# Kernel tuning notes

Measured on AMD Instinct MI355X. Metric: run time of the kernel, lower is better.

The kernel has to match this reference:

```python
import jax, jax.numpy as jnp
import numpy as np

UNITS = 50
FEAT = 128
OUT = 74


def _glorot(key, shape):
    fan_in, fan_out = shape[0], shape[1]
    lim = (6.0 / (fan_in + fan_out)) ** 0.5
    return jax.random.uniform(key, shape, jnp.float32, -lim, lim)


def setup_inputs() -> dict:
    key = jax.random.key(0)
    ks = jax.random.split(key, 8)
    x = jax.random.normal(ks[0], (1024, 256, FEAT), jnp.float32)
    # forward-direction LSTM params (keras gate order: i, f, c, o)
    W_f = _glorot(ks[1], (FEAT, 4 * UNITS))
    U_f = _glorot(ks[2], (UNITS, 4 * UNITS))
    b_f = jnp.zeros((4 * UNITS,), jnp.float32).at[UNITS:2 * UNITS].set(1.0)  # unit forget bias
    # backward-direction LSTM params
    W_b = _glorot(ks[3], (FEAT, 4 * UNITS))
    U_b = _glorot(ks[4], (UNITS, 4 * UNITS))
    b_b = jnp.zeros((4 * UNITS,), jnp.float32).at[UNITS:2 * UNITS].set(1.0)
    # dense softmax head: [2*UNITS, OUT]
    W_d = _glorot(ks[5], (2 * UNITS, OUT))
    b_d = jnp.zeros((OUT,), jnp.float32)
    return {"x": x, "W_f": W_f, "U_f": U_f, "b_f": b_f,
            "W_b": W_b, "U_b": U_b, "b_b": b_b, "W_d": W_d, "b_d": b_d}


def _lstm_last(x, W, U, b):
    # x: [B, T, F]; relu cell activation, sigmoid recurrent activation (keras defaults except activation)
    B = x.shape[0]
    h0 = jnp.zeros((B, UNITS), x.dtype)
    c0 = jnp.zeros((B, UNITS), x.dtype)
    # precompute input projections for all timesteps: [T, B, 4U]
    zx = jnp.einsum('btf,fg->tbg', x, W) + b

    def step(carry, zx_t):
        h, c = carry
        z = zx_t + h @ U
        i, f, g, o = jnp.split(z, 4, axis=-1)
        i = jax.nn.sigmoid(i)
        f = jax.nn.sigmoid(f)
        g = jax.nn.relu(g)
        o = jax.nn.sigmoid(o)
        c = f * c + i * g
        h = o * jax.nn.relu(c)
        return (h, c), None

    (h, c), _ = jax.lax.scan(step, (h0, c0), zx)
    return h  # last hidden state, [B, UNITS]


def reference(x, W_f, U_f, b_f, W_b, U_b, b_b, W_d, b_d):
    h_fwd = _lstm_last(x, W_f, U_f, b_f)
    h_bwd = _lstm_last(x[:, ::-1, :], W_b, U_b, b_b)
    h = jnp.concatenate([h_fwd, h_bwd], axis=-1)  # [B, 100]
    logits = h @ W_d + b_d
    return jax.nn.softmax(logits, axis=-1)  # [B, 74]
```

## Files before the change

### kernel.cpp

```cpp
#include <hip/hip_runtime.h>
#include <hip/hip_bf16.h>
#include <math.h>

#define T_SEQ 256
#define FEAT  128
#define UNITS 50
#define NG    200
#define OUTD  74
#define BATCH 1024
#define NPAD  224
#define WPLANE (NPAD * FEAT)

typedef __attribute__((ext_vector_type(8)))  short bf16x8;
typedef __attribute__((ext_vector_type(16))) float f32x16;

__device__ __forceinline__ unsigned short f2bf(float f) {
    unsigned u = __float_as_uint(f);
    return (unsigned short)((u + 0x7fffu + ((u >> 16) & 1u)) >> 16);
}
__device__ __forceinline__ float bf2f(unsigned short h) {
    return __uint_as_float(((unsigned)h) << 16);
}
__device__ __forceinline__ float sigf(float x) {
    return __builtin_amdgcn_rcpf(1.f + __expf(-x));
}

__global__ __launch_bounds__(256) void prep_w(
    const float* __restrict__ Wf, const float* __restrict__ Wb,
    unsigned short* __restrict__ Wt)
{
    const int idx = blockIdx.x * 256 + threadIdx.x;
    const int dir = blockIdx.y;
    const int col = idx >> 7, k = idx & 127;
    const float* W = dir ? Wb : Wf;
    const float v = (col < NG) ? W[k * NG + col] : 0.f;
    const unsigned short hi = f2bf(v);
    const unsigned short lo = f2bf(v - bf2f(hi));
    Wt[(size_t)(dir * 2 + 0) * WPLANE + idx] = hi;
    Wt[(size_t)(dir * 2 + 1) * WPLANE + idx] = lo;
}

__global__ __launch_bounds__(256) void prep_x(
    const float* __restrict__ x,
    unsigned short* __restrict__ xh, unsigned short* __restrict__ xl,
    int Tc, int lTc, int t0, int n4)
{
    const int stride = gridDim.x * blockDim.x;
    for (int e4 = blockIdx.x * blockDim.x + threadIdx.x; e4 < n4; e4 += stride) {
        const int row = e4 >> 5, k4 = e4 & 31;
        const int b = row >> lTc, ti = row & (Tc - 1);
        const float4 v = *(const float4*)(x + (((size_t)(b * T_SEQ + t0 + ti)) << 7) + (k4 << 2));
        ushort4 hi, lo;
        hi.x = f2bf(v.x); lo.x = f2bf(v.x - bf2f(hi.x));
        hi.y = f2bf(v.y); lo.y = f2bf(v.y - bf2f(hi.y));
        hi.z = f2bf(v.z); lo.z = f2bf(v.z - bf2f(hi.z));
        hi.w = f2bf(v.w); lo.w = f2bf(v.w - bf2f(hi.w));
        *(ushort4*)(xh + ((size_t)e4 << 2)) = hi;
        *(ushort4*)(xl + ((size_t)e4 << 2)) = lo;
    }
}

__global__ __launch_bounds__(448, 2) void proj_mfma(
    const unsigned short* __restrict__ xfh, const unsigned short* __restrict__ xfl,
    const unsigned short* __restrict__ xbh, const unsigned short* __restrict__ xbl,
    const unsigned short* __restrict__ Wt,
    float* __restrict__ zf, float* __restrict__ zb,
    int mpb, int nMT)
{
    const int dir = blockIdx.y;
    const unsigned short* __restrict__ Ah_p = dir ? xbh : xfh;
    const unsigned short* __restrict__ Al_p = dir ? xbl : xfl;
    float* __restrict__ z = dir ? zb : zf;
    const unsigned short* __restrict__ Wth = Wt + (size_t)(dir * 2) * WPLANE;
    const unsigned short* __restrict__ Wtl = Wth + WPLANE;

    const int l    = threadIdx.x & 63;
    const int wv   = threadIdx.x >> 6;
    const int ln   = l & 31;
    const int half = l >> 5;
    const int col  = wv * 32 + ln;

    bf16x8 Bh[8], Bl[8];
#pragma unroll
    for (int ks = 0; ks < 8; ++ks) {
        const size_t wo = (size_t)col * 128 + ks * 16 + half * 8;
        Bh[ks] = *(const bf16x8*)(Wth + wo);
        Bl[ks] = *(const bf16x8*)(Wtl + wo);
    }
    const bool colOK = (col < NG);

    int mt = blockIdx.x * mpb;
    bf16x8 Ah[8], Al[8], Ah2[8], Al2[8];
    {
        const size_t ab = ((size_t)(mt * 32 + ln)) << 7;
#pragma unroll
        for (int ks = 0; ks < 8; ++ks) {
            Ah[ks] = *(const bf16x8*)(Ah_p + ab + ks * 16 + half * 8);
            Al[ks] = *(const bf16x8*)(Al_p + ab + ks * 16 + half * 8);
        }
    }

    for (int i = 0; i < mpb; ++i) {
        const int mtn = (i + 1 < mpb) ? (mt + 1) : mt;
        const size_t an = ((size_t)(mtn * 32 + ln)) << 7;
#pragma unroll
        for (int ks = 0; ks < 8; ++ks) {
            Ah2[ks] = *(const bf16x8*)(Ah_p + an + ks * 16 + half * 8);
            Al2[ks] = *(const bf16x8*)(Al_p + an + ks * 16 + half * 8);
        }

        f32x16 acc = {};
#pragma unroll
        for (int ks = 0; ks < 8; ++ks) {
            acc = __builtin_amdgcn_mfma_f32_32x32x16_bf16(Ah[ks], Bh[ks], acc, 0, 0, 0);
            acc = __builtin_amdgcn_mfma_f32_32x32x16_bf16(Ah[ks], Bl[ks], acc, 0, 0, 0);
            acc = __builtin_amdgcn_mfma_f32_32x32x16_bf16(Al[ks], Bh[ks], acc, 0, 0, 0);
        }

        if (colOK) {
            float* zp = z + (size_t)(mt * 32 + half * 4) * NG + col;
#pragma unroll
            for (int r = 0; r < 16; ++r) {
                const int row = (r & 3) + ((r >> 2) << 3);
                zp[(size_t)row * NG] = acc[r];
            }
        }
#pragma unroll
        for (int ks = 0; ks < 8; ++ks) { Ah[ks] = Ah2[ks]; Al[ks] = Al2[ks]; }
        ++mt;
    }
}

__global__ __launch_bounds__(256, 4) void rec3(
    const float* __restrict__ zf, const float* __restrict__ zb,
    const float* __restrict__ Uf, const float* __restrict__ Ub,
    const float* __restrict__ bf_, const float* __restrict__ bb_,
    float* __restrict__ hF, float* __restrict__ cF,
    float* __restrict__ hB, float* __restrict__ cB,
    int Tc, int first)
{
    const int j = threadIdx.x;
    const int b = blockIdx.x, dir = blockIdx.y;
    const float* __restrict__ z    = dir ? zb : zf;
    const float* __restrict__ U    = dir ? Ub : Uf;
    const float* __restrict__ bias = dir ? bb_ : bf_;
    float* __restrict__ hS = dir ? hB : hF;
    float* __restrict__ cS = dir ? cB : cF;
    const bool act = (j < NG);
    const bool isg = (j >= 100) && (j < 150);

    float Ur[50];
#pragma unroll
    for (int k = 0; k < 50; ++k) Ur[k] = act ? U[k * NG + j] : 0.f;
    const float bj = act ? bias[j] : 0.f;

    __shared__ __align__(16) float hsh[52];
    __shared__ float gsh[NG];

    float c = 0.f;
    if (j < 50) {
        c      = first ? 0.f : cS[b * 50 + j];
        hsh[j] = first ? 0.f : hS[b * 50 + j];
    }
    if (j >= 50 && j < 52) hsh[j] = 0.f;
    __syncthreads();

    const int stp = dir ? -1 : 1;
    int ti = dir ? (Tc - 1) : 0;
    const float* __restrict__ zr = z + (size_t)b * Tc * NG;

    float zc = act ? zr[(size_t)ti * NG + j] : 0.f;

    for (int tt = 0; tt < Tc; ++tt) {
        const int tin = ti + stp;
        float zn = 0.f;
        if (tt + 1 < Tc && act) zn = zr[(size_t)tin * NG + j];

        float a = zc + bj;
#pragma unroll
        for (int k4 = 0; k4 < 12; ++k4) {
            const float4 h4 = *(const float4*)(hsh + (k4 << 2));
            a = fmaf(h4.x, Ur[k4 * 4 + 0], a);
            a = fmaf(h4.y, Ur[k4 * 4 + 1], a);
            a = fmaf(h4.z, Ur[k4 * 4 + 2], a);
            a = fmaf(h4.w, Ur[k4 * 4 + 3], a);
        }
        {
            const float2 h2 = *(const float2*)(hsh + 48);
            a = fmaf(h2.x, Ur[48], a);
            a = fmaf(h2.y, Ur[49], a);
        }

        const float s = sigf(a);
        const float r = fmaxf(a, 0.f);
        if (act) gsh[j] = isg ? r : s;
        __syncthreads();

        if (j < 50) {
            const float gi = gsh[j];
            const float gf = gsh[50 + j];
            const float gg = gsh[100 + j];
            const float go = gsh[150 + j];
            c = fmaf(gf, c, gi * gg);
            hsh[j] = go * fmaxf(c, 0.f);
        }
        __syncthreads();

        zc = zn;
        ti = tin;
    }

    if (j < 50) {
        hS[b * 50 + j] = hsh[j];
        cS[b * 50 + j] = c;
    }
}

__global__ __launch_bounds__(128) void head_kernel(
    const float* __restrict__ hF, const float* __restrict__ hB,
    const float* __restrict__ Wd, const float* __restrict__ bd,
    float* __restrict__ out)
{
    const int b   = blockIdx.x;
    const int tid = threadIdx.x;
    __shared__ float hsh[100];
    __shared__ float red[128];

    if (tid < 50) {
        hsh[tid]      = hF[b * 50 + tid];
        hsh[50 + tid] = hB[b * 50 + tid];
    }
    __syncthreads();

    float logit = -INFINITY;
    if (tid < OUTD) {
        float acc = bd[tid];
#pragma unroll 4
        for (int k = 0; k < 100; ++k) acc = fmaf(hsh[k], Wd[k * OUTD + tid], acc);
        logit = acc;
    }
    red[tid] = logit;
    __syncthreads();
    for (int s = 64; s > 0; s >>= 1) {
        if (tid < s) red[tid] = fmaxf(red[tid], red[tid + s]);
        __syncthreads();
    }
    const float m = red[0];
    __syncthreads();
    const float e = (tid < OUTD) ? expf(logit - m) : 0.f;
    red[tid] = e;
    __syncthreads();
    for (int s = 64; s > 0; s >>= 1) {
        if (tid < s) red[tid] += red[tid + s];
        __syncthreads();
    }
    if (tid < OUTD) out[b * OUTD + tid] = e / red[0];
}

extern "C" void kernel_launch(void* const* d_in, const int* in_sizes, int n_in,
                              void* d_out, int out_size, void* d_ws, size_t ws_size,
                              hipStream_t stream)
{
    const float* x  = (const float*)d_in[0];
    const float* Wf = (const float*)d_in[1];
    const float* Uf = (const float*)d_in[2];
    const float* bf = (const float*)d_in[3];
    const float* Wb = (const float*)d_in[4];
    const float* Ub = (const float*)d_in[5];
    const float* bb = (const float*)d_in[6];
    const float* Wd = (const float*)d_in[7];
    const float* bd = (const float*)d_in[8];
    float* out = (float*)d_out;

    auto aln = [](size_t v) { return (v + 255) & ~(size_t)255; };

    int Tc = T_SEQ;
    bool shx = true;
    for (;;) {
        shx = (Tc == T_SEQ);
        const size_t zsz = aln((size_t)BATCH * Tc * NG * 4);
        const size_t xsz = aln((size_t)BATCH * Tc * FEAT * 2);
        const size_t need = 2 * zsz + (shx ? 2 : 4) * xsz
                          + aln(4 * WPLANE * 2) + aln(4ull * BATCH * UNITS * 4);
        if (need <= ws_size || Tc == 8) break;
        Tc >>= 1;
    }
    const int lTc = __builtin_ctz((unsigned)Tc);
    const size_t zsz = aln((size_t)BATCH * Tc * NG * 4);
    const size_t xsz = aln((size_t)BATCH * Tc * FEAT * 2);

    char* p = (char*)d_ws;
    float* zf = (float*)p; p += zsz;
    float* zb = (float*)p; p += zsz;
    unsigned short* xfh = (unsigned short*)p; p += xsz;
    unsigned short* xfl = (unsigned short*)p; p += xsz;
    unsigned short* xbh = xfh;
    unsigned short* xbl = xfl;
    if (!shx) {
        xbh = (unsigned short*)p; p += xsz;
        xbl = (unsigned short*)p; p += xsz;
    }
    unsigned short* Wt = (unsigned short*)p; p += aln(4 * WPLANE * 2);
    float* st = (float*)p;
    float* hF = st;
    float* cF = st + BATCH * UNITS;
    float* hB = st + 2 * BATCH * UNITS;
    float* cB = st + 3 * BATCH * UNITS;

    prep_w<<<dim3(WPLANE / 256, 2), 256, 0, stream>>>(Wf, Wb, Wt);

    const int n4  = BATCH * Tc * 32;
    const int nMT = BATCH * Tc / 32;
    const int NBLK = (nMT < 512) ? nMT : 512;
    const int mpb = nMT / NBLK;
    const int nc  = T_SEQ / Tc;

    for (int c = 0; c < nc; ++c) {
        const int t0f = c * Tc;
        const int t0b = T_SEQ - (c + 1) * Tc;
        prep_x<<<2048, 256, 0, stream>>>(x, xfh, xfl, Tc, lTc, t0f, n4);
        if (!shx)
            prep_x<<<2048, 256, 0, stream>>>(x, xbh, xbl, Tc, lTc, t0b, n4);
        proj_mfma<<<dim3(NBLK, 2), 448, 0, stream>>>(
            xfh, xfl, xbh, xbl, Wt, zf, zb, mpb, nMT);
        rec3<<<dim3(BATCH, 2), 256, 0, stream>>>(
            zf, zb, Uf, Ub, bf, bb, hF, cF, hB, cB, Tc, c == 0);
    }
    head_kernel<<<BATCH, 128, 0, stream>>>(hF, hB, Wd, bd, out);
}
```

Baseline: 944.3 us.

## Batch recurrent LSTM step over 32 sequences using split-bf16 MFMA

The recurrent kernel is replaced: each block now handles 32 batch rows per direction instead of one. The h·U product runs on 32x32x16 bf16 MFMAs, using a hi/lo split with three products per k-slice to stay close to fp32 accuracy. U is pre-split into bf16 planes by a new prep kernel, and h is kept in LDS as bf16 hi/lo pairs. This removes per-sequence scalar FMA loops and amortises U loads, but the grid shrinks to 64 blocks, which leaves most CUs idle during the latency-bound time loop.

```diff
diff --git a/kernel.cpp b/kernel.cpp
--- a/kernel.cpp
+++ b/kernel.cpp
@@ -10,6 +10,11 @@
 #define BATCH 1024
 #define NPAD  224
 #define WPLANE (NPAD * FEAT)
+#define G32   32
+#define KP    64
+#define HL    68
+#define GSW   224
+#define UPLANE (NPAD * KP)
 
 typedef __attribute__((ext_vector_type(8)))  short bf16x8;
 typedef __attribute__((ext_vector_type(16))) float f32x16;
@@ -38,6 +43,21 @@
     const unsigned short lo = f2bf(v - bf2f(hi));
     Wt[(size_t)(dir * 2 + 0) * WPLANE + idx] = hi;
     Wt[(size_t)(dir * 2 + 1) * WPLANE + idx] = lo;
+}
+
+__global__ __launch_bounds__(256) void prep_u(
+    const float* __restrict__ Uf, const float* __restrict__ Ub,
+    unsigned short* __restrict__ Ut)
+{
+    const int idx = blockIdx.x * 256 + threadIdx.x;
+    const int dir = blockIdx.y;
+    const int col = idx >> 6, k = idx & 63;
+    const float* U = dir ? Ub : Uf;
+    const float v = (col < NG && k < UNITS) ? U[k * NG + col] : 0.f;
+    const unsigned short hi = f2bf(v);
+    const unsigned short lo = f2bf(v - bf2f(hi));
+    Ut[(size_t)(dir * 2 + 0) * UPLANE + idx] = hi;
+    Ut[(size_t)(dir * 2 + 1) * UPLANE + idx] = lo;
 }
 
 __global__ __launch_bounds__(256) void prep_x(
@@ -131,88 +151,156 @@
     }
 }
 
-__global__ __launch_bounds__(256, 4) void rec3(
+__global__ __launch_bounds__(512, 1) void rec4(
     const float* __restrict__ zf, const float* __restrict__ zb,
-    const float* __restrict__ Uf, const float* __restrict__ Ub,
+    const unsigned short* __restrict__ Ut,
     const float* __restrict__ bf_, const float* __restrict__ bb_,
     float* __restrict__ hF, float* __restrict__ cF,
     float* __restrict__ hB, float* __restrict__ cB,
     int Tc, int first)
 {
-    const int j = threadIdx.x;
-    const int b = blockIdx.x, dir = blockIdx.y;
+    const int tid = threadIdx.x;
+    const int dir = blockIdx.y;
+    const int b0  = blockIdx.x * G32;
     const float* __restrict__ z    = dir ? zb : zf;
-    const float* __restrict__ U    = dir ? Ub : Uf;
     const float* __restrict__ bias = dir ? bb_ : bf_;
+    const unsigned short* __restrict__ Uth = Ut + (size_t)(dir * 2) * UPLANE;
+    const unsigned short* __restrict__ Utl = Uth + UPLANE;
     float* __restrict__ hS = dir ? hB : hF;
     float* __restrict__ cS = dir ? cB : cF;
-    const bool act = (j < NG);
-    const bool isg = (j >= 100) && (j < 150);
-
-    float Ur[50];
-#pragma unroll
-    for (int k = 0; k < 50; ++k) Ur[k] = act ? U[k * NG + j] : 0.f;
-    const float bj = act ? bias[j] : 0.f;
-
-    __shared__ __align__(16) float hsh[52];
-    __shared__ float gsh[NG];
-
-    float c = 0.f;
-    if (j < 50) {
-        c      = first ? 0.f : cS[b * 50 + j];
-        hsh[j] = first ? 0.f : hS[b * 50 + j];
-    }
-    if (j >= 50 && j < 52) hsh[j] = 0.f;
-    __syncthreads();
-
+
+    __shared__ unsigned short h_hi[G32][HL];
+    __shared__ unsigned short h_lo[G32][HL];
+    __shared__ float gsh[G32][GSW];
+
+    const int l    = tid & 63;
+    const int wv   = tid >> 6;
+    const int ln   = l & 31;
+    const int half = l >> 5;
+    const int col  = wv * 32 + ln;
+    const bool mf  = (wv < 7);
+    const bool cOK = mf && (col < NG);
+    const bool isg = (col >= 100) && (col < 150);
+    const float bcol = cOK ? bias[col] : 0.f;
+
+    bf16x8 Bh0 = {}, Bh1 = {}, Bh2 = {}, Bh3 = {};
+    bf16x8 Bl0 = {}, Bl1 = {}, Bl2 = {}, Bl3 = {};
+    if (mf) {
+        const size_t ob = (size_t)col * KP + half * 8;
+        Bh0 = *(const bf16x8*)(Uth + ob);      Bl0 = *(const bf16x8*)(Utl + ob);
+        Bh1 = *(const bf16x8*)(Uth + ob + 16); Bl1 = *(const bf16x8*)(Utl + ob + 16);
+        Bh2 = *(const bf16x8*)(Uth + ob + 32); Bl2 = *(const bf16x8*)(Utl + ob + 32);
+        Bh3 = *(const bf16x8*)(Uth + ob + 48); Bl3 = *(const bf16x8*)(Utl + ob + 48);
+    }
+
+    for (int idx = tid; idx < G32 * HL; idx += 512) {
+        ((unsigned short*)h_hi)[idx] = 0;
+        ((unsigned short*)h_lo)[idx] = 0;
+    }
+    __syncthreads();
+    float creg[4] = {0.f, 0.f, 0.f, 0.f};
+#pragma unroll
+    for (int i = 0; i < 4; ++i) {
+        const int m = tid + i * 512;
+        if (m < G32 * UNITS && !first) {
+            const int r = m / UNITS, u = m % UNITS;
+            creg[i] = cS[(b0 + r) * UNITS + u];
+            const float hv = hS[(b0 + r) * UNITS + u];
+            const unsigned short hi = f2bf(hv);
+            h_hi[r][u] = hi;
+            h_lo[r][u] = f2bf(hv - bf2f(hi));
+        }
+    }
+    __syncthreads();
+
+    unsigned zrb[16];
+    if (cOK) {
+#pragma unroll
+        for (int i = 0; i < 16; ++i) {
+            const int row = (i & 3) + ((i >> 2) << 3) + half * 4;
+            zrb[i] = (unsigned)(((b0 + row) * Tc) * NG + col);
+        }
+    }
     const int stp = dir ? -1 : 1;
-    int ti = dir ? (Tc - 1) : 0;
-    const float* __restrict__ zr = z + (size_t)b * Tc * NG;
-
-    float zc = act ? zr[(size_t)ti * NG + j] : 0.f;
+    int ti = dir ? Tc - 1 : 0;
+    float zc[16], zn[16];
+#pragma unroll
+    for (int i = 0; i < 16; ++i) { zc[i] = 0.f; zn[i] = 0.f; }
+    if (cOK) {
+#pragma unroll
+        for (int i = 0; i < 16; ++i) zc[i] = z[zrb[i] + (unsigned)(ti * NG)];
+    }
 
     for (int tt = 0; tt < Tc; ++tt) {
         const int tin = ti + stp;
-        float zn = 0.f;
-        if (tt + 1 < Tc && act) zn = zr[(size_t)tin * NG + j];
-
-        float a = zc + bj;
-#pragma unroll
-        for (int k4 = 0; k4 < 12; ++k4) {
-            const float4 h4 = *(const float4*)(hsh + (k4 << 2));
-            a = fmaf(h4.x, Ur[k4 * 4 + 0], a);
-            a = fmaf(h4.y, Ur[k4 * 4 + 1], a);
-            a = fmaf(h4.z, Ur[k4 * 4 + 2], a);
-            a = fmaf(h4.w, Ur[k4 * 4 + 3], a);
-        }
-        {
-            const float2 h2 = *(const float2*)(hsh + 48);
-            a = fmaf(h2.x, Ur[48], a);
-            a = fmaf(h2.y, Ur[49], a);
-        }
-
-        const float s = sigf(a);
-        const float r = fmaxf(a, 0.f);
-        if (act) gsh[j] = isg ? r : s;
+        if (tt + 1 < Tc && cOK) {
+#pragma unroll
+            for (int i = 0; i < 16; ++i) zn[i] = z[zrb[i] + (unsigned)(tin * NG)];
+        }
+
+        f32x16 a1 = {}, a2 = {};
+        if (mf) {
+            const int ho = half * 8;
+            const bf16x8 Ah0 = *(const bf16x8*)(&h_hi[ln][ho]);
+            const bf16x8 Al0 = *(const bf16x8*)(&h_lo[ln][ho]);
+            const bf16x8 Ah1 = *(const bf16x8*)(&h_hi[ln][16 + ho]);
+            const bf16x8 Al1 = *(const bf16x8*)(&h_lo[ln][16 + ho]);
+            const bf16x8 Ah2 = *(const bf16x8*)(&h_hi[ln][32 + ho]);
+            const bf16x8 Al2 = *(const bf16x8*)(&h_lo[ln][32 + ho]);
+            const bf16x8 Ah3 = *(const bf16x8*)(&h_hi[ln][48 + ho]);
+            const bf16x8 Al3 = *(const bf16x8*)(&h_lo[ln][48 + ho]);
+            a1 = __builtin_amdgcn_mfma_f32_32x32x16_bf16(Ah0, Bh0, a1, 0, 0, 0);
+            a2 = __builtin_amdgcn_mfma_f32_32x32x16_bf16(Ah2, Bh2, a2, 0, 0, 0);
+            a1 = __builtin_amdgcn_mfma_f32_32x32x16_bf16(Ah0, Bl0, a1, 0, 0, 0);
+            a2 = __builtin_amdgcn_mfma_f32_32x32x16_bf16(Ah2, Bl2, a2, 0, 0, 0);
+            a1 = __builtin_amdgcn_mfma_f32_32x32x16_bf16(Al0, Bh0, a1, 0, 0, 0);
+            a2 = __builtin_amdgcn_mfma_f32_32x32x16_bf16(Al2, Bh2, a2, 0, 0, 0);
+            a1 = __builtin_amdgcn_mfma_f32_32x32x16_bf16(Ah1, Bh1, a1, 0, 0, 0);
+            a2 = __builtin_amdgcn_mfma_f32_32x32x16_bf16(Ah3, Bh3, a2, 0, 0, 0);
+            a1 = __builtin_amdgcn_mfma_f32_32x32x16_bf16(Ah1, Bl1, a1, 0, 0, 0);
+            a2 = __builtin_amdgcn_mfma_f32_32x32x16_bf16(Ah3, Bl3, a2, 0, 0, 0);
+            a1 = __builtin_amdgcn_mfma_f32_32x32x16_bf16(Al1, Bh1, a1, 0, 0, 0);
+            a2 = __builtin_amdgcn_mfma_f32_32x32x16_bf16(Al3, Bh3, a2, 0, 0, 0);
+#pragma unroll
+            for (int i = 0; i < 16; ++i) {
+                const int row = (i & 3) + ((i >> 2) << 3) + half * 4;
+                const float a = a1[i] + a2[i] + zc[i] + bcol;
+                gsh[row][col] = isg ? fmaxf(a, 0.f) : sigf(a);
+            }
+        }
         __syncthreads();
-
-        if (j < 50) {
-            const float gi = gsh[j];
-            const float gf = gsh[50 + j];
-            const float gg = gsh[100 + j];
-            const float go = gsh[150 + j];
-            c = fmaf(gf, c, gi * gg);
-            hsh[j] = go * fmaxf(c, 0.f);
+#pragma unroll
+        for (int i = 0; i < 4; ++i) {
+            const int m = tid + i * 512;
+            if (m < G32 * UNITS) {
+                const int r = m / UNITS, u = m % UNITS;
+                const float gi = gsh[r][u];
+                const float gf = gsh[r][50 + u];
+                const float gg = gsh[r][100 + u];
+                const float go = gsh[r][150 + u];
+                creg[i] = fmaf(gf, creg[i], gi * gg);
+                const float h = go * fmaxf(creg[i], 0.f);
+                const unsigned short hi = f2bf(h);
+                h_hi[r][u] = hi;
+                h_lo[r][u] = f2bf(h - bf2f(hi));
+            }
         }
         __syncthreads();
-
-        zc = zn;
+        if (cOK) {
+#pragma unroll
+            for (int i = 0; i < 16; ++i) zc[i] = zn[i];
+        }
         ti = tin;
     }
 
-    if (j < 50) {
-        hS[b * 50 + j] = hsh[j];
-        cS[b * 50 + j] = c;
+#pragma unroll
+    for (int i = 0; i < 4; ++i) {
+        const int m = tid + i * 512;
+        if (m < G32 * UNITS) {
+            const int r = m / UNITS, u = m % UNITS;
+            hS[(b0 + r) * UNITS + u] = bf2f(h_hi[r][u]) + bf2f(h_lo[r][u]);
+            cS[(b0 + r) * UNITS + u] = creg[i];
+        }
     }
 }
 
@@ -281,7 +369,8 @@
         const size_t zsz = aln((size_t)BATCH * Tc * NG * 4);
         const size_t xsz = aln((size_t)BATCH * Tc * FEAT * 2);
         const size_t need = 2 * zsz + (shx ? 2 : 4) * xsz
-                          + aln(4 * WPLANE * 2) + aln(4ull * BATCH * UNITS * 4);
+                          + aln(4 * WPLANE * 2) + aln(4 * UPLANE * 2)
+                          + aln(4ull * BATCH * UNITS * 4);
         if (need <= ws_size || Tc == 8) break;
         Tc >>= 1;
     }
@@ -301,6 +390,7 @@
         xbl = (unsigned short*)p; p += xsz;
     }
     unsigned short* Wt = (unsigned short*)p; p += aln(4 * WPLANE * 2);
+    unsigned short* Uu = (unsigned short*)p; p += aln(4 * UPLANE * 2);
     float* st = (float*)p;
     float* hF = st;
     float* cF = st + BATCH * UNITS;
@@ -308,6 +398,7 @@
     float* cB = st + 3 * BATCH * UNITS;
 
     prep_w<<<dim3(WPLANE / 256, 2), 256, 0, stream>>>(Wf, Wb, Wt);
+    prep_u<<<dim3(UPLANE / 256, 2), 256, 0, stream>>>(Uf, Ub, Uu);
 
     const int n4  = BATCH * Tc * 32;
     const int nMT = BATCH * Tc / 32;
@@ -323,8 +414,8 @@
             prep_x<<<2048, 256, 0, stream>>>(x, xbh, xbl, Tc, lTc, t0b, n4);
         proj_mfma<<<dim3(NBLK, 2), 448, 0, stream>>>(
             xfh, xfl, xbh, xbl, Wt, zf, zb, mpb, nMT);
-        rec3<<<dim3(BATCH, 2), 256, 0, stream>>>(
-            zf, zb, Uf, Ub, bf, bb, hF, cF, hB, cB, Tc, c == 0);
+        rec4<<<dim3(BATCH / G32, 2), 512, 0, stream>>>(
+            zf, zb, Uu, bf, bb, hF, cF, hB, cB, Tc, c == 0);
     }
     head_kernel<<<BATCH, 128, 0, stream>>>(hF, hB, Wd, bd, out);
 }
```

New measurement: 1.223 ms. +29.5%, slower.

## Process four batch rows per block in LSTM recurrence with U in shared memory

Applied to the files above, without the earlier changes.

The recurrent kernel now handles four batch sequences per workgroup instead of one. Each thread computes gate pre-activations for four rows and reuses every U value read from shared memory across them. U moves from a 50-float per-thread register array into a padded shared-memory tile, and the grid shrinks by four. This spreads each step's per-block barriers and weight reads over four sequences. In exchange there are 4x fewer blocks, fewer waves to hide latency, and LDS reads of U on every step.

```diff
diff --git a/kernel.cpp b/kernel.cpp
--- a/kernel.cpp
+++ b/kernel.cpp
@@ -10,6 +10,7 @@
 #define BATCH 1024
 #define NPAD  224
 #define WPLANE (NPAD * FEAT)
+#define R4    4
 
 typedef __attribute__((ext_vector_type(8)))  short bf16x8;
 typedef __attribute__((ext_vector_type(16))) float f32x16;
@@ -131,7 +132,7 @@
     }
 }
 
-__global__ __launch_bounds__(256, 4) void rec3(
+__global__ __launch_bounds__(256) void rec5(
     const float* __restrict__ zf, const float* __restrict__ zb,
     const float* __restrict__ Uf, const float* __restrict__ Ub,
     const float* __restrict__ bf_, const float* __restrict__ bb_,
@@ -139,80 +140,112 @@
     float* __restrict__ hB, float* __restrict__ cB,
     int Tc, int first)
 {
-    const int j = threadIdx.x;
-    const int b = blockIdx.x, dir = blockIdx.y;
+    const int tid = threadIdx.x;
+    const int dir = blockIdx.y;
+    const int b0  = blockIdx.x * R4;
     const float* __restrict__ z    = dir ? zb : zf;
     const float* __restrict__ U    = dir ? Ub : Uf;
     const float* __restrict__ bias = dir ? bb_ : bf_;
     float* __restrict__ hS = dir ? hB : hF;
     float* __restrict__ cS = dir ? cB : cF;
-    const bool act = (j < NG);
+
+    __shared__ float Us[52][NG];
+    __shared__ __align__(16) float hsh[R4][52];
+    __shared__ float gsh[R4][NG];
+
+    const bool act = (tid < NG);
+    const int  j   = tid;
     const bool isg = (j >= 100) && (j < 150);
-
-    float Ur[50];
-#pragma unroll
-    for (int k = 0; k < 50; ++k) Ur[k] = act ? U[k * NG + j] : 0.f;
     const float bj = act ? bias[j] : 0.f;
 
-    __shared__ __align__(16) float hsh[52];
-    __shared__ float gsh[NG];
-
-    float c = 0.f;
-    if (j < 50) {
-        c      = first ? 0.f : cS[b * 50 + j];
-        hsh[j] = first ? 0.f : hS[b * 50 + j];
-    }
-    if (j >= 50 && j < 52) hsh[j] = 0.f;
+    if (act) {
+#pragma unroll
+        for (int k = 0; k < UNITS; ++k) Us[k][j] = U[k * NG + j];
+        Us[50][j] = 0.f;
+        Us[51][j] = 0.f;
+    }
+
+    const int ur = tid / UNITS;
+    const int uu = tid - ur * UNITS;
+    float creg = 0.f;
+    if (tid < R4 * UNITS) {
+        creg = first ? 0.f : cS[(b0 + ur) * UNITS + uu];
+        hsh[ur][uu] = first ? 0.f : hS[(b0 + ur) * UNITS + uu];
+    }
+    if (tid < R4 * 2) hsh[tid >> 1][50 + (tid & 1)] = 0.f;
     __syncthreads();
 
     const int stp = dir ? -1 : 1;
-    int ti = dir ? (Tc - 1) : 0;
-    const float* __restrict__ zr = z + (size_t)b * Tc * NG;
-
-    float zc = act ? zr[(size_t)ti * NG + j] : 0.f;
+    int ti = dir ? Tc - 1 : 0;
+    int zofs[R4];
+#pragma unroll
+    for (int r = 0; r < R4; ++r)
+        zofs[r] = ((b0 + r) * Tc) * NG + (act ? j : 0);
+
+    float zc[R4] = {0.f, 0.f, 0.f, 0.f};
+    float zn[R4];
+    if (act) {
+#pragma unroll
+        for (int r = 0; r < R4; ++r) zc[r] = z[zofs[r] + ti * NG];
+    }
 
     for (int tt = 0; tt < Tc; ++tt) {
         const int tin = ti + stp;
-        float zn = 0.f;
-        if (tt + 1 < Tc && act) zn = zr[(size_t)tin * NG + j];
-
-        float a = zc + bj;
-#pragma unroll
-        for (int k4 = 0; k4 < 12; ++k4) {
-            const float4 h4 = *(const float4*)(hsh + (k4 << 2));
-            a = fmaf(h4.x, Ur[k4 * 4 + 0], a);
-            a = fmaf(h4.y, Ur[k4 * 4 + 1], a);
-            a = fmaf(h4.z, Ur[k4 * 4 + 2], a);
-            a = fmaf(h4.w, Ur[k4 * 4 + 3], a);
-        }
-        {
-            const float2 h2 = *(const float2*)(hsh + 48);
-            a = fmaf(h2.x, Ur[48], a);
-            a = fmaf(h2.y, Ur[49], a);
-        }
-
-        const float s = sigf(a);
-        const float r = fmaxf(a, 0.f);
-        if (act) gsh[j] = isg ? r : s;
+#pragma unroll
+        for (int r = 0; r < R4; ++r) zn[r] = 0.f;
+        if (tt + 1 < Tc && act) {
+#pragma unroll
+            for (int r = 0; r < R4; ++r) zn[r] = z[zofs[r] + tin * NG];
+        }
+
+        float a0 = zc[0] + bj, a1 = zc[1] + bj;
+        float a2 = zc[2] + bj, a3 = zc[3] + bj;
+#pragma unroll
+        for (int k4 = 0; k4 < 13; ++k4) {
+            const float4 h0 = *(const float4*)&hsh[0][k4 * 4];
+            const float4 h1 = *(const float4*)&hsh[1][k4 * 4];
+            const float4 h2 = *(const float4*)&hsh[2][k4 * 4];
+            const float4 h3 = *(const float4*)&hsh[3][k4 * 4];
+            const float u0 = Us[k4 * 4 + 0][j];
+            const float u1 = Us[k4 * 4 + 1][j];
+            const float u2 = Us[k4 * 4 + 2][j];
+            const float u3 = Us[k4 * 4 + 3][j];
+            a0 = fmaf(h0.x, u0, a0); a1 = fmaf(h1.x, u0, a1);
+            a2 = fmaf(h2.x, u0, a2); a3 = fmaf(h3.x, u0, a3);
+            a0 = fmaf(h0.y, u1, a0); a1 = fmaf(h1.y, u1, a1);
+            a2 = fmaf(h2.y, u1, a2); a3 = fmaf(h3.y, u1, a3);
+            a0 = fmaf(h0.z, u2, a0); a1 = fmaf(h1.z, u2, a1);
+            a2 = fmaf(h2.z, u2, a2); a3 = fmaf(h3.z, u2, a3);
+            a0 = fmaf(h0.w, u3, a0); a1 = fmaf(h1.w, u3, a1);
+            a2 = fmaf(h2.w, u3, a2); a3 = fmaf(h3.w, u3, a3);
+        }
+
+        if (act) {
+            gsh[0][j] = isg ? fmaxf(a0, 0.f) : sigf(a0);
+            gsh[1][j] = isg ? fmaxf(a1, 0.f) : sigf(a1);
+            gsh[2][j] = isg ? fmaxf(a2, 0.f) : sigf(a2);
+            gsh[3][j] = isg ? fmaxf(a3, 0.f) : sigf(a3);
+        }
         __syncthreads();
 
-        if (j < 50) {
-            const float gi = gsh[j];
-            const float gf = gsh[50 + j];
-            const float gg = gsh[100 + j];
-            const float go = gsh[150 + j];
-            c = fmaf(gf, c, gi * gg);
-            hsh[j] = go * fmaxf(c, 0.f);
+        if (tid < R4 * UNITS) {
+            const float gi = gsh[ur][uu];
+            const float gf = gsh[ur][50 + uu];
+            const float gg = gsh[ur][100 + uu];
+            const float go = gsh[ur][150 + uu];
+            creg = fmaf(gf, creg, gi * gg);
+            hsh[ur][uu] = go * fmaxf(creg, 0.f);
         }
         __syncthreads();
 
-        zc = zn;
+#pragma unroll
+        for (int r = 0; r < R4; ++r) zc[r] = zn[r];
         ti = tin;
     }
 
-    if (j < 50) {
-        hS[b * 50 + j] = hsh[j];
-        cS[b * 50 + j] = c;
+    if (tid < R4 * UNITS) {
+        hS[(b0 + ur) * UNITS + uu] = hsh[ur][uu];
+        cS[(b0 + ur) * UNITS + uu] = creg;
     }
 }
 
@@ -281,7 +314,8 @@
         const size_t zsz = aln((size_t)BATCH * Tc * NG * 4);
         const size_t xsz = aln((size_t)BATCH * Tc * FEAT * 2);
         const size_t need = 2 * zsz + (shx ? 2 : 4) * xsz
-                          + aln(4 * WPLANE * 2) + aln(4ull * BATCH * UNITS * 4);
+                          + aln(4 * WPLANE * 2)
+                          + aln(4ull * BATCH * UNITS * 4);
         if (need <= ws_size || Tc == 8) break;
         Tc >>= 1;
     }
@@ -323,7 +357,7 @@
             prep_x<<<2048, 256, 0, stream>>>(x, xbh, xbl, Tc, lTc, t0b, n4);
         proj_mfma<<<dim3(NBLK, 2), 448, 0, stream>>>(
             xfh, xfl, xbh, xbl, Wt, zf, zb, mpb, nMT);
-        rec3<<<dim3(BATCH, 2), 256, 0, stream>>>(
+        rec5<<<dim3(BATCH / R4, 2), 256, 0, stream>>>(
             zf, zb, Uf, Ub, bf, bb, hF, cF, hB, cB, Tc, c == 0);
     }
     head_kernel<<<BATCH, 128, 0, stream>>>(hF, hB, Wd, bd, out);
```

Result: slower. 1.508 ms (+59.6%).
